# Kernel optimization log

Measured on AMD Instinct MI355X. Metric: run time of the kernel, lower is better.

The kernel has to match this reference:

```python
import jax, jax.numpy as jnp
import numpy as np
from jax.scipy.special import i0

IM_SIZE = (256, 256)
GRID_SIZE = (512, 512)
NUMPOINTS = 6
OS = GRID_SIZE[0] / IM_SIZE[0]
# Beatty et al. optimal Kaiser-Bessel shape parameter
BETA = float(np.pi * np.sqrt((NUMPOINTS / OS) ** 2 * (OS - 0.5) ** 2 - 0.8))


def _apod_1d(N, G):
    # 1/FT(kb kernel) scaling coefficients (de-apodization), static numpy
    x = np.arange(N) - N / 2.0
    arg = np.pi * NUMPOINTS * x / G
    t = BETA ** 2 - arg ** 2  # > 0 for this config
    ph = np.sinh(np.sqrt(t)) / np.sqrt(t)
    return (1.0 / ph).astype(np.float32)


def _kb(u):
    # Kaiser-Bessel interpolation kernel, support |u| <= NUMPOINTS/2
    x = 2.0 * u / NUMPOINTS
    t = 1.0 - x * x
    inside = t > 0
    t = jnp.where(inside, t, 0.0)
    return jnp.where(inside, i0(BETA * jnp.sqrt(t)), 0.0)


def setup_inputs():
    key = jax.random.key(0)
    k1, k2, k3 = jax.random.split(key, 3)
    B, M = 8, 131072
    image = jax.random.normal(k1, (B,) + IM_SIZE, dtype=jnp.float32)
    ktraj = (jax.random.uniform(k2, (B, 2, M), dtype=jnp.float32) * 2.0 - 1.0) * jnp.pi
    dcf = jax.random.uniform(k3, (B, M), dtype=jnp.float32)
    return {"image": image, "ktraj": ktraj, "dcf": dcf}


def _nufft(image, ktraj, dcf):
    B = image.shape[0]
    N1, N2 = IM_SIZE
    G1, G2 = GRID_SIZE
    J = NUMPOINTS
    # 1) de-apodization (scaling coefficients), separable per-dim
    a1 = jnp.asarray(_apod_1d(N1, G1))
    a2 = jnp.asarray(_apod_1d(N2, G2))
    img = image.astype(jnp.complex64) * (a1[:, None] * a2[None, :])
    # 2) centered zero-pad to oversampled grid, FFT with DC at bin 0
    p1, p2 = (G1 - N1) // 2, (G2 - N2) // 2
    grid = jnp.zeros((B, G1, G2), dtype=jnp.complex64).at[:, p1:p1 + N1, p2:p2 + N2].set(img)
    kgrid = jnp.fft.fft2(jnp.fft.ifftshift(grid, axes=(1, 2)))
    # 3) KB interpolation (gather) at non-uniform points
    tm1 = ktraj[:, 0] * (G1 / (2.0 * jnp.pi))  # (B,M) in grid units
    tm2 = ktraj[:, 1] * (G2 / (2.0 * jnp.pi))
    offs = jnp.arange(J, dtype=jnp.float32) - (J // 2 - 1)  # [-2..3]
    g1 = jnp.floor(tm1)[..., None] + offs  # (B,M,J) neighbor coords
    g2 = jnp.floor(tm2)[..., None] + offs
    w1 = _kb(tm1[..., None] - g1)
    w2 = _kb(tm2[..., None] - g2)
    i1 = jnp.mod(g1.astype(jnp.int32), G1)
    i2 = jnp.mod(g2.astype(jnp.int32), G2)
    lin = (i1[..., :, None] * G2 + i2[..., None, :]).reshape(B, -1)  # (B, M*J*J)
    vals = jnp.take_along_axis(kgrid.reshape(B, -1), lin, axis=1).reshape(B, -1, J, J)
    w = (w1[..., :, None] * w2[..., None, :]).astype(jnp.complex64)
    kdata = jnp.sum(vals * w, axis=(-1, -2))  # (B,M) complex
    kdata = kdata * dcf
    return jnp.stack([kdata.real, kdata.imag], axis=0)  # (2,B,M) float32


def reference(image, ktraj, dcf):
    return _nufft(image, ktraj, dcf)
```

## Files before the change

### kernel.cpp

```cpp
#include <hip/hip_runtime.h>
#include <math.h>

#define GSZ 512
#define NSZ 256
#define NBATCH 8
#define MPTS 131072
#define PI_F 3.14159265358979f
#define BETA_F 13.8551004f
#define BETA2_F (BETA_F * BETA_F)
#define RSQ2 0.70710678f
#define PADIDX(i) ((i) + ((i) >> 3))
#define LUTN 768


__device__ __forceinline__ float apod(int i) {
    float x = (float)(i - 128);
    float arg = PI_F * 6.0f * x * (1.0f / 512.0f);
    float t = BETA2_F - arg * arg;
    float st = sqrtf(t);
    return st / sinhf(st);
}

__device__ __forceinline__ float bessi0(float x) {
    float ax = fabsf(x);
    if (ax < 3.75f) {
        float y = ax * (1.0f / 3.75f);
        y *= y;
        return 1.0f + y * (3.5156229f + y * (3.0899424f + y * (1.2067492f
             + y * (0.2659732f + y * (0.0360768f + y * 0.0045813f)))));
    } else {
        float y = 3.75f / ax;
        float p = 0.39894228f + y * (0.01328592f + y * (0.00225319f + y * (-0.00157565f
             + y * (0.00916281f + y * (-0.02057706f + y * (0.02635537f + y * (-0.01647633f
             + y * 0.00392377f)))))));
        return p * __expf(ax) * rsqrtf(ax);
    }
}

__device__ __forceinline__ float kblut(const float* __restrict__ lut, float u) {
    float s = u * u;
    float p = s * ((float)LUTN / 9.0f);
    p = fminf(p, (float)(LUTN - 1));
    int i = (int)p;
    float f = p - (float)i;
    float w = fmaf(f, lut[i + 1] - lut[i], lut[i]);
    return (s < 9.0f) ? w : 0.f;
}

__device__ __forceinline__ float2 cadd(float2 a, float2 b){ return make_float2(a.x+b.x, a.y+b.y); }
__device__ __forceinline__ float2 csub(float2 a, float2 b){ return make_float2(a.x-b.x, a.y-b.y); }
__device__ __forceinline__ float2 cmul(float2 a, float2 b){ return make_float2(a.x*b.x-a.y*b.y, a.x*b.y+a.y*b.x); }
__device__ __forceinline__ float2 mul_negi(float2 a){ return make_float2(a.y, -a.x); }
__device__ __forceinline__ float2 mul_posi(float2 a){ return make_float2(-a.y, a.x); }
__device__ __forceinline__ float2 mul_w81(float2 a){ return make_float2(RSQ2*(a.x+a.y), RSQ2*(a.y-a.x)); }
__device__ __forceinline__ float2 mul_w83(float2 a){ return make_float2(RSQ2*(a.y-a.x), -RSQ2*(a.x+a.y)); }

__device__ __forceinline__ void dft8_combine(float2 E0, float2 E1, float2 E2, float2 E3,
                                             float2 O0, float2 O1, float2 O2, float2 O3,
                                             float2* y) {
    float2 c1 = mul_w81(O1), c2 = mul_negi(O2), c3 = mul_w83(O3);
    y[0] = cadd(E0, O0); y[4] = csub(E0, O0);
    y[1] = cadd(E1, c1); y[5] = csub(E1, c1);
    y[2] = cadd(E2, c2); y[6] = csub(E2, c2);
    y[3] = cadd(E3, c3); y[7] = csub(E3, c3);
}

__device__ __forceinline__ void dft8(const float2* x, float2* y) {
    float2 a0=x[0], a1=x[2], a2=x[4], a3=x[6];
    float2 b0=x[1], b1=x[3], b2=x[5], b3=x[7];
    float2 ta0=cadd(a0,a2), ta1=csub(a0,a2), ta2=cadd(a1,a3), ta3=csub(a1,a3);
    float2 E0=cadd(ta0,ta2), E2=csub(ta0,ta2);
    float2 E1=cadd(ta1, mul_negi(ta3)), E3=cadd(ta1, mul_posi(ta3));
    float2 tb0=cadd(b0,b2), tb1=csub(b0,b2), tb2=cadd(b1,b3), tb3=csub(b1,b3);
    float2 O0=cadd(tb0,tb2), O2=csub(tb0,tb2);
    float2 O1=cadd(tb1, mul_negi(tb3)), O3=cadd(tb1, mul_posi(tb3));
    dft8_combine(E0,E1,E2,E3,O0,O1,O2,O3,y);
}

__device__ __forceinline__ void dft8_pruned(float2 x0, float2 x1, float2 x6, float2 x7, float2* y) {
    float2 E0 = cadd(x0, x6), E2 = csub(x0, x6);
    float2 E1 = cadd(x0, mul_posi(x6)), E3 = cadd(x0, mul_negi(x6));
    float2 O0 = cadd(x1, x7), O2 = csub(x1, x7);
    float2 O1 = cadd(x1, mul_posi(x7)), O3 = cadd(x1, mul_negi(x7));
    dft8_combine(E0,E1,E2,E3,O0,O1,O2,O3,y);
}

template<int S>
__device__ __forceinline__ void twiddle8(int t, float2* y) {
    if (S < 2) {
        int j = (S == 0) ? t : (t >> 3);
        const float scale = (S == 0) ? (-2.0f*PI_F/512.0f) : (-2.0f*PI_F/64.0f);
        float theta = scale * (float)j;
        float sn, cs;
        __sincosf(theta, &sn, &cs);
        float2 w = make_float2(cs, sn), wq = w;
        y[1] = cmul(y[1], wq);
        #pragma unroll
        for (int q = 2; q < 8; ++q) { wq = cmul(wq, w); y[q] = cmul(y[q], wq); }
    }
}

__global__ __launch_bounds__(256) void pass1_rowfft(const float* __restrict__ image,
                                                    float2* __restrict__ T) {
    __shared__ float2 sm[2][4][578];
    int tid = threadIdx.x;
    int r = tid >> 6, t = tid & 63;
    int blk = blockIdx.x;
    int b = blk & 7;
    int g = blk >> 3;
    int rp = (g << 2) + r;
    int y = (rp < 128) ? rp : (rp + 256);
    int iy = (y < 128) ? (y + 128) : (y - 384);
    float ay = apod(iy);
    const float* irow = image + ((size_t)(b * NSZ + iy)) * NSZ;

    float2 y8[8];
    {
        int ix0 = t + 128, ix1 = t + 192, ix6 = t, ix7 = t + 64;
        float2 x0 = make_float2(irow[ix0] * ay * apod(ix0), 0.f);
        float2 x1 = make_float2(irow[ix1] * ay * apod(ix1), 0.f);
        float2 x6 = make_float2(irow[ix6] * ay * apod(ix6), 0.f);
        float2 x7 = make_float2(irow[ix7] * ay * apod(ix7), 0.f);
        dft8_pruned(x0, x1, x6, x7, y8);
        twiddle8<0>(t, y8);
    }
    float2* A  = sm[0][r];
    float2* Bf = sm[1][r];
    #pragma unroll
    for (int q = 0; q < 8; ++q) A[PADIDX((t << 3) + q)] = y8[q];
    __syncthreads();
    {
        float2 x[8];
        #pragma unroll
        for (int p = 0; p < 8; ++p) x[p] = A[PADIDX(t + (p << 6))];
        dft8(x, y8);
        twiddle8<1>(t, y8);
        int j = t >> 3, k = t & 7, base = k + (j << 6);
        #pragma unroll
        for (int q = 0; q < 8; ++q) Bf[PADIDX(base + (q << 3))] = y8[q];
    }
    __syncthreads();
    {
        float2 x[8];
        #pragma unroll
        for (int p = 0; p < 8; ++p) x[p] = Bf[PADIDX(t + (p << 6))];
        dft8(x, y8);
        float2* Trow = T + (((size_t)(b << 8) + rp) << 9);
        #pragma unroll
        for (int q = 0; q < 8; ++q) Trow[t + (q << 6)] = y8[q];
    }
}

__global__ __launch_bounds__(256) void pass2_colfft(const float2* __restrict__ T,
                                                    float2* __restrict__ kgrid) {
    __shared__ float2 B[8][578];
    int tid = threadIdx.x;
    int blk = blockIdx.x;
    int b = blk & 7;
    int colbase = (blk >> 3) << 3;
    const float2* Tb = T + ((size_t)b << 17);
    float2* Kb = kgrid + ((size_t)b << 18);

    {
        int c = tid & 7, r0 = tid >> 3;
        #pragma unroll
        for (int k = 0; k < 8; ++k) {
            int rr = r0 + (k << 5);
            B[c][PADIDX(rr)] = Tb[((size_t)rr << 9) + colbase + c];
        }
    }
    __syncthreads();
    int t = tid & 63;
    int c0 = tid >> 6;
    float2 ya[8], yb[8];
    {
        float2* Ba = B[c0];
        float2* Bb = B[c0 + 4];
        float2 a0 = Ba[PADIDX(t)],   a1 = Ba[PADIDX(t + 64)];
        float2 a6 = Ba[PADIDX(t + 128)], a7 = Ba[PADIDX(t + 192)];
        float2 b0 = Bb[PADIDX(t)],   b1 = Bb[PADIDX(t + 64)];
        float2 b6 = Bb[PADIDX(t + 128)], b7 = Bb[PADIDX(t + 192)];
        dft8_pruned(a0, a1, a6, a7, ya); twiddle8<0>(t, ya);
        dft8_pruned(b0, b1, b6, b7, yb); twiddle8<0>(t, yb);
    }
    __syncthreads();
    #pragma unroll
    for (int q = 0; q < 8; ++q) {
        B[c0][PADIDX((t << 3) + q)]     = ya[q];
        B[c0 + 4][PADIDX((t << 3) + q)] = yb[q];
    }
    __syncthreads();
    {
        float2 xa[8], xb[8];
        #pragma unroll
        for (int p = 0; p < 8; ++p) { xa[p] = B[c0][PADIDX(t + (p << 6))]; xb[p] = B[c0 + 4][PADIDX(t + (p << 6))]; }
        dft8(xa, ya); twiddle8<1>(t, ya);
        dft8(xb, yb); twiddle8<1>(t, yb);
    }
    __syncthreads();
    {
        int j = t >> 3, k = t & 7, base = k + (j << 6);
        #pragma unroll
        for (int q = 0; q < 8; ++q) {
            B[c0][PADIDX(base + (q << 3))]     = ya[q];
            B[c0 + 4][PADIDX(base + (q << 3))] = yb[q];
        }
    }
    __syncthreads();
    {
        float2 xa[8], xb[8];
        #pragma unroll
        for (int p = 0; p < 8; ++p) { xa[p] = B[c0][PADIDX(t + (p << 6))]; xb[p] = B[c0 + 4][PADIDX(t + (p << 6))]; }
        dft8(xa, ya);
        dft8(xb, yb);
    }
    __syncthreads();
    #pragma unroll
    for (int q = 0; q < 8; ++q) {
        B[c0][PADIDX(t + (q << 6))]     = ya[q];
        B[c0 + 4][PADIDX(t + (q << 6))] = yb[q];
    }
    __syncthreads();
    {
        int c = tid & 7, r0 = tid >> 3;
        #pragma unroll
        for (int k = 0; k < 16; ++k) {
            int rr = r0 + (k << 5);
            Kb[((size_t)rr << 9) + colbase + c] = B[c][PADIDX(rr)];
        }
    }
}

__global__ __launch_bounds__(256) void interp_kb(const float* __restrict__ ktraj,
                                                 const float* __restrict__ dcf,
                                                 const float2* __restrict__ kgrid,
                                                 float* __restrict__ out) {
    __shared__ float lut[LUTN + 1];
    int tid = threadIdx.x;
    for (int i = tid; i <= LUTN; i += 256) {
        float s = (float)i * (9.0f / (float)LUTN);
        float tt = fmaxf(1.0f - s * (1.0f / 9.0f), 0.f);
        lut[i] = bessi0(BETA_F * sqrtf(tt));
    }
    __syncthreads();

    int blk = blockIdx.x;
    int b = blk & 7;
    int gb = blk >> 3;
    int j = tid & 7;
    int gloc = tid >> 3;
    int lane = tid & 63;
    int gbase = lane & 56;

    const float SCALE = (float)GSZ / (2.0f * PI_F);
    const float2* Kb = kgrid + ((size_t)b << 18);
    const float* kt1 = ktraj + ((size_t)(b * 2)) * MPTS;
    const float* kt2 = kt1 + MPTS;
    const float* dcfb = dcf + ((size_t)b << 17);
    float* out_re = out + ((size_t)b << 17);
    float* out_im = out_re + (size_t)NBATCH * MPTS;

    int m0 = (gb << 9) + gloc;
    #pragma unroll 2
    for (int it = 0; it < 16; ++it) {
        int m = m0 + (it << 5);
        float tm1 = kt1[m] * SCALE;
        float tm2 = kt2[m] * SCALE;
        float f1 = floorf(tm1), f2 = floorf(tm2);
        int if1 = (int)f1, if2 = (int)f2;

        float w2_own = kblut(lut, tm2 - f2 - (float)(j - 2));
        int   i2_own = (if2 + j - 2) & 511;
        float w1_own = kblut(lut, tm1 - f1 - (float)(j - 2));

        float s_re = 0.f, s_im = 0.f;
        #pragma unroll
        for (int a = 0; a < 6; ++a) {
            int i1a = (if1 + a - 2) & 511;
            float w1a = __shfl(w1_own, gbase + a, 64);
            float2 v = Kb[((size_t)i1a << 9) + i2_own];
            s_re = fmaf(w1a, v.x, s_re);
            s_im = fmaf(w1a, v.y, s_im);
        }
        float p_re = w2_own * s_re;
        float p_im = w2_own * s_im;
        #pragma unroll
        for (int d = 1; d < 8; d <<= 1) {
            p_re += __shfl_xor(p_re, d, 64);
            p_im += __shfl_xor(p_im, d, 64);
        }
        float dd = dcfb[m];
        if (j == 0) out_re[m] = p_re * dd;
        if (j == 1) out_im[m] = p_im * dd;
    }
}


extern "C" void kernel_launch(void* const* d_in, const int* in_sizes, int n_in,
                              void* d_out, int out_size, void* d_ws, size_t ws_size,
                              hipStream_t stream) {
    const float* image = (const float*)d_in[0];
    const float* ktraj = (const float*)d_in[1];
    const float* dcf   = (const float*)d_in[2];
    float* out = (float*)d_out;

    float2* T     = (float2*)d_ws;
    float2* kgrid = T + (size_t)NBATCH * 256 * GSZ;

    pass1_rowfft<<<NBATCH * 64, 256, 0, stream>>>(image, T);
    pass2_colfft<<<NBATCH * 64, 256, 0, stream>>>(T, kgrid);
    interp_kb<<<NBATCH * 256, 256, 0, stream>>>(ktraj, dcf, kgrid, out);
}
```

Before: 133.1 us.

## Use 4 lanes per point with paired-column loads, DPP reductions, analytic KB weights

The interpolation kernel drops from 8 threads per sample to 4. Each thread now loads two adjacent grid columns as one 16-byte load, aligned to an even column (so 8 columns cover the 6-wide window), and accumulates both. Cross-lane weight broadcasts and the final reduction use quad DPP moves instead of generic shuffles. The shared-memory Bessel LUT and its setup barrier are replaced by an inline asymptotic exp/rsqrt approximation of I0, which may lose accuracy for small arguments near the kernel edge.

```diff
diff --git a/kernel.cpp b/kernel.cpp
--- a/kernel.cpp
+++ b/kernel.cpp
@@ -10,7 +10,6 @@
 #define BETA2_F (BETA_F * BETA_F)
 #define RSQ2 0.70710678f
 #define PADIDX(i) ((i) + ((i) >> 3))
-#define LUTN 768
 
 
 __device__ __forceinline__ float apod(int i) {
@@ -21,31 +20,23 @@
     return st / sinhf(st);
 }
 
-__device__ __forceinline__ float bessi0(float x) {
-    float ax = fabsf(x);
-    if (ax < 3.75f) {
-        float y = ax * (1.0f / 3.75f);
-        y *= y;
-        return 1.0f + y * (3.5156229f + y * (3.0899424f + y * (1.2067492f
-             + y * (0.2659732f + y * (0.0360768f + y * 0.0045813f)))));
-    } else {
-        float y = 3.75f / ax;
-        float p = 0.39894228f + y * (0.01328592f + y * (0.00225319f + y * (-0.00157565f
-             + y * (0.00916281f + y * (-0.02057706f + y * (0.02635537f + y * (-0.01647633f
-             + y * 0.00392377f)))))));
-        return p * __expf(ax) * rsqrtf(ax);
-    }
-}
-
-__device__ __forceinline__ float kblut(const float* __restrict__ lut, float u) {
-    float s = u * u;
-    float p = s * ((float)LUTN / 9.0f);
-    p = fminf(p, (float)(LUTN - 1));
-    int i = (int)p;
-    float f = p - (float)i;
-    float w = fmaf(f, lut[i + 1] - lut[i], lut[i]);
-    return (s < 9.0f) ? w : 0.f;
-}
+__device__ __forceinline__ float kbw(float u) {
+    float t = 1.0f - u * u * (1.0f / 9.0f);
+    float x = BETA_F * sqrtf(fmaxf(t, 0.0f));
+    float xc = fmaxf(x, 0.35f);
+    float r = __builtin_amdgcn_rcpf(xc);
+    float poly = 1.0f + r * (0.125f + r * 0.0703125f);
+    float w = __expf(xc) * __builtin_amdgcn_rsqf(6.2831853f * xc) * poly;
+    return (t > 0.0f) ? w : 0.0f;
+}
+
+template<int CTRL>
+__device__ __forceinline__ float qdpp(float v) {
+    int r = __builtin_amdgcn_mov_dpp(__float_as_int(v), CTRL, 0xF, 0xF, true);
+    return __int_as_float(r);
+}
+
+struct __align__(8) F4 { float x, y, z, w; };
 
 __device__ __forceinline__ float2 cadd(float2 a, float2 b){ return make_float2(a.x+b.x, a.y+b.y); }
 __device__ __forceinline__ float2 csub(float2 a, float2 b){ return make_float2(a.x-b.x, a.y-b.y); }
@@ -235,22 +226,12 @@
                                                  const float* __restrict__ dcf,
                                                  const float2* __restrict__ kgrid,
                                                  float* __restrict__ out) {
-    __shared__ float lut[LUTN + 1];
     int tid = threadIdx.x;
-    for (int i = tid; i <= LUTN; i += 256) {
-        float s = (float)i * (9.0f / (float)LUTN);
-        float tt = fmaxf(1.0f - s * (1.0f / 9.0f), 0.f);
-        lut[i] = bessi0(BETA_F * sqrtf(tt));
-    }
-    __syncthreads();
-
     int blk = blockIdx.x;
     int b = blk & 7;
     int gb = blk >> 3;
-    int j = tid & 7;
-    int gloc = tid >> 3;
-    int lane = tid & 63;
-    int gbase = lane & 56;
+    int j = tid & 3;
+    int q = tid >> 2;
 
     const float SCALE = (float)GSZ / (2.0f * PI_F);
     const float2* Kb = kgrid + ((size_t)b << 18);
@@ -260,35 +241,47 @@
     float* out_re = out + ((size_t)b << 17);
     float* out_im = out_re + (size_t)NBATCH * MPTS;
 
-    int m0 = (gb << 9) + gloc;
+    int m0 = (gb << 9) + q;
     #pragma unroll 2
-    for (int it = 0; it < 16; ++it) {
-        int m = m0 + (it << 5);
+    for (int it = 0; it < 8; ++it) {
+        int m = m0 + (it << 6);
         float tm1 = kt1[m] * SCALE;
         float tm2 = kt2[m] * SCALE;
         float f1 = floorf(tm1), f2 = floorf(tm2);
         int if1 = (int)f1, if2 = (int)f2;
-
-        float w2_own = kblut(lut, tm2 - f2 - (float)(j - 2));
-        int   i2_own = (if2 + j - 2) & 511;
-        float w1_own = kblut(lut, tm1 - f1 - (float)(j - 2));
-
-        float s_re = 0.f, s_im = 0.f;
-        #pragma unroll
-        for (int a = 0; a < 6; ++a) {
-            int i1a = (if1 + a - 2) & 511;
-            float w1a = __shfl(w1_own, gbase + a, 64);
-            float2 v = Kb[((size_t)i1a << 9) + i2_own];
-            s_re = fmaf(w1a, v.x, s_re);
-            s_im = fmaf(w1a, v.y, s_im);
+        int e0 = (if2 - 2) & ~1;
+
+        float u2 = tm2 - (float)(e0 + 2 * j);
+        float w2a = kbw(u2);
+        float w2b = kbw(u2 - 1.0f);
+        int cpair = (e0 + 2 * j) & 511;
+
+        float fr1 = tm1 - f1;
+        float w1A = kbw(fr1 - (float)(j - 2));
+        float w1B = kbw(fr1 - (float)(j + 2));
+
+        float c0re = 0.f, c0im = 0.f, c1re = 0.f, c1im = 0.f;
+        #define KB_ROW(a, W, CTRL)                                            \
+        {                                                                     \
+            float w1a = qdpp<CTRL>(W);                                        \
+            int rowb = (if1 + (a) - 2) & 511;                                 \
+            F4 v = *reinterpret_cast<const F4*>(Kb + ((size_t)rowb << 9) + cpair); \
+            c0re = fmaf(w1a, v.x, c0re); c0im = fmaf(w1a, v.y, c0im);         \
+            c1re = fmaf(w1a, v.z, c1re); c1im = fmaf(w1a, v.w, c1im);         \
         }
-        float p_re = w2_own * s_re;
-        float p_im = w2_own * s_im;
-        #pragma unroll
-        for (int d = 1; d < 8; d <<= 1) {
-            p_re += __shfl_xor(p_re, d, 64);
-            p_im += __shfl_xor(p_im, d, 64);
-        }
+        KB_ROW(0, w1A, 0x00)
+        KB_ROW(1, w1A, 0x55)
+        KB_ROW(2, w1A, 0xAA)
+        KB_ROW(3, w1A, 0xFF)
+        KB_ROW(4, w1B, 0x00)
+        KB_ROW(5, w1B, 0x55)
+        #undef KB_ROW
+
+        float p_re = fmaf(w2a, c0re, w2b * c1re);
+        float p_im = fmaf(w2a, c0im, w2b * c1im);
+        p_re += qdpp<0xB1>(p_re);  p_re += qdpp<0x4E>(p_re);
+        p_im += qdpp<0xB1>(p_im);  p_im += qdpp<0x4E>(p_im);
+
         float dd = dcfb[m];
         if (j == 0) out_re[m] = p_re * dd;
         if (j == 1) out_im[m] = p_im * dd;
```

After: 128.5 us. 1.04x faster.
